# Kernel optimization log

Hardware: AMD Instinct MI355X
Metric: run time of the kernel (lower is better)

Reference implementation:

```python
import jax, jax.numpy as jnp
import numpy as np

B = 131072
INPUT_SIZE = 128
HIDDEN_SIZE = 128


def setup_inputs() -> dict:
    key = jax.random.key(0)
    ks = jax.random.split(key, 11)
    stdv = 1.0 / (HIDDEN_SIZE ** 0.5)

    def unif(k, shape):
        return jax.random.uniform(k, shape, dtype=jnp.float32, minval=-stdv, maxval=stdv)

    return {
        "x_t": jax.random.normal(ks[0], (B, INPUT_SIZE), dtype=jnp.float32),
        "h_prev": jax.random.normal(ks[1], (B, HIDDEN_SIZE), dtype=jnp.float32),
        "Wz": unif(ks[2], (INPUT_SIZE, HIDDEN_SIZE)),
        "Uz": unif(ks[3], (HIDDEN_SIZE, HIDDEN_SIZE)),
        "bz": unif(ks[4], (HIDDEN_SIZE,)),
        "Wr": unif(ks[5], (INPUT_SIZE, HIDDEN_SIZE)),
        "Ur": unif(ks[6], (HIDDEN_SIZE, HIDDEN_SIZE)),
        "br": unif(ks[7], (HIDDEN_SIZE,)),
        "Wh": unif(ks[8], (INPUT_SIZE, HIDDEN_SIZE)),
        "Uh": unif(ks[9], (HIDDEN_SIZE, HIDDEN_SIZE)),
        "bh": unif(ks[10], (HIDDEN_SIZE,)),
    }


def reference(x_t, h_prev, Wz, Uz, bz, Wr, Ur, br, Wh, Uh, bh):
    # Fuse the three input-side and two hidden-side GEMMs by concatenating weights.
    W = jnp.concatenate([Wz, Wr, Wh], axis=1)        # [I, 3H]
    U = jnp.concatenate([Uz, Ur], axis=1)            # [H, 2H]
    xw = x_t @ W                                     # [B, 3H]
    hu = h_prev @ U                                  # [B, 2H]
    H = bz.shape[0]
    z_t = jax.nn.sigmoid(xw[:, :H] + hu[:, :H] + bz)
    r_t = jax.nn.sigmoid(xw[:, H:2 * H] + hu[:, H:] + br)
    h_cand = jnp.tanh(xw[:, 2 * H:] + (r_t * h_prev) @ Uh + bh)
    h_t = (1.0 - z_t) * h_prev + z_t * h_cand
    return h_t
```

## Files before the change

kernel.cpp:

```cpp
#include <hip/hip_runtime.h>
#include <hip/hip_bf16.h>

typedef __attribute__((ext_vector_type(8))) short bf16x8;
typedef __attribute__((ext_vector_type(4))) float f32x4;

#define GRU_B 131072
#define BM 32
#define TPB 8
#define NBLK (GRU_B / (BM * TPB))

static __device__ __forceinline__ ushort f2bf(float f) {
  union { float f; unsigned u; } v; v.f = f;
  unsigned r = v.u + 0x7FFFu + ((v.u >> 16) & 1u);
  return (ushort)(r >> 16);
}
static __device__ __forceinline__ float bf2f(ushort u) {
  union { unsigned u; float f; } v; v.u = ((unsigned)u) << 16;
  return v.f;
}
static __device__ __forceinline__ unsigned pk2(float a, float b) {
  float2 t; t.x = a; t.y = b;
  __hip_bfloat162 r = __float22bfloat162_rn(t);
  union { __hip_bfloat162 b; unsigned u; } cv; cv.b = r;
  return cv.u;
}
static __device__ __forceinline__ float fsig(float x) {
  return __builtin_amdgcn_rcpf(1.0f + __expf(-x));
}
static __device__ __forceinline__ float ftanh(float x) {
  return 1.0f - 2.0f * __builtin_amdgcn_rcpf(1.0f + __expf(2.0f * x));
}
static __device__ __forceinline__ int swz(int row, int cbyte) {
  return (row * 256 + cbyte) ^ ((row & 7) << 4) ^ ((row & 8) << 2);
}

#define BARRIER() do {                                       \
  asm volatile("s_waitcnt lgkmcnt(0)" ::: "memory");         \
  __builtin_amdgcn_s_barrier();                              \
  asm volatile("" ::: "memory");                             \
} while (0)

__global__ void wtrans_kernel(const float* __restrict__ wz, const float* __restrict__ uz,
                              const float* __restrict__ wr, const float* __restrict__ ur,
                              const float* __restrict__ wh, const float* __restrict__ uh,
                              ushort* __restrict__ outw) {
  int f = blockIdx.x * 256 + threadIdx.x;
  int mat = f >> 14;
  int rem = f & 16383;
  int chunk = rem >> 9;
  int lane = (rem >> 3) & 63;
  int e = rem & 7;
  int cb = chunk >> 2, k0b = chunk & 3;
  int n = cb * 16 + (lane & 15);
  int k = k0b * 32 + (lane >> 4) * 8 + e;
  const float* src = (mat == 0) ? wz : (mat == 1) ? uz : (mat == 2) ? wr
                   : (mat == 3) ? ur : (mat == 4) ? wh : uh;
  outw[f] = f2bf(src[k * 128 + n]);
}

#define MFMA __builtin_amdgcn_mfma_f32_16x16x32_bf16

__global__ __launch_bounds__(512, 2) void gru_kernel(
    const float* __restrict__ x, const float* __restrict__ hprev,
    const ushort* __restrict__ wt,
    const float* __restrict__ bz, const float* __restrict__ br,
    const float* __restrict__ bh, float* __restrict__ out) {
  __shared__ __align__(16) char smem[65536];

  const int tid = threadIdx.x;
  const int lane = tid & 63;
  const int wid = tid >> 6;
  const int l15 = lane & 15;
  const int q = lane >> 4;
  const int n0 = wid * 16;

  const float4 brv = *(const float4*)(br + n0 + q * 4);
  const float4 bzv = *(const float4*)(bz + n0 + q * 4);
  const float4 bhv = *(const float4*)(bh + n0 + q * 4);
  const f32x4 brv4 = {brv.x, brv.y, brv.z, brv.w};
  const f32x4 bzv4 = {bzv.x, bzv.y, bzv.z, bzv.w};
  const f32x4 bhv4 = {bhv.x, bhv.y, bhv.z, bhv.w};

  const ushort* wlane = wt + (lane << 3);
  bf16x8 W[6][4];
#pragma unroll
  for (int mat = 0; mat < 6; ++mat)
#pragma unroll
    for (int kb = 0; kb < 4; ++kb)
      W[mat][kb] = *(const bf16x8*)(wlane + ((((mat << 3) + wid) << 2) + kb) * 512);

  auto ldsA = [&](const char* base, int mr, int k0) -> bf16x8 {
    int row = mr * 16 + l15;
    return *(const bf16x8*)(base + swz(row, (k0 + q * 8) * 2));
  };

  const long tile0 = (long)blockIdx.x * TPB;
  const float4* xg = (const float4*)x;
  const float4* hg = (const float4*)hprev;

  const int r0 = tid >> 5, cb0 = (tid & 31) << 3;
  const int bo0 = swz(r0, cb0), bo1 = swz(r0 + 16, cb0);
  const int go0 = swz(l15, (n0 + q * 4) * 2);
  const int go1 = swz(16 + l15, (n0 + q * 4) * 2);

  auto stage = [&](char* S, const float4& a0, const float4& a1,
                   const float4& b0, const float4& b1) {
    uint2 v;
    v.x = pk2(a0.x, a0.y); v.y = pk2(a0.z, a0.w); *(uint2*)(S + bo0) = v;
    v.x = pk2(a1.x, a1.y); v.y = pk2(a1.z, a1.w); *(uint2*)(S + bo1) = v;
    v.x = pk2(b0.x, b0.y); v.y = pk2(b0.z, b0.w); *(uint2*)(S + 8192 + bo0) = v;
    v.x = pk2(b1.x, b1.y); v.y = pk2(b1.z, b1.w); *(uint2*)(S + 8192 + bo1) = v;
  };

  float4 px0, px1, ph0, ph1;
  {
    long toff = tile0 * 1024;
    px0 = xg[toff + tid]; px1 = xg[toff + 512 + tid];
    ph0 = hg[toff + tid]; ph1 = hg[toff + 512 + tid];
    stage(smem, px0, px1, ph0, ph1);
    if (TPB > 1) {
      toff += 1024;
      px0 = xg[toff + tid]; px1 = xg[toff + 512 + tid];
      ph0 = hg[toff + tid]; ph1 = hg[toff + 512 + tid];
    }
  }
  BARRIER();

  for (int t = 0; t < TPB; ++t) {
    char* Scur = smem + (t % 3) * 16384;
    char* RHc  = smem + 49152 + (t & 1) * 8192;
    const long row0 = (tile0 + t) * BM;

    if (t + 1 < TPB) stage(smem + ((t + 1) % 3) * 16384, px0, px1, ph0, ph1);

    if (t + 2 < TPB) {
      long toff = (tile0 + t + 2) * 1024;
      px0 = xg[toff + tid]; px1 = xg[toff + 512 + tid];
      ph0 = hg[toff + tid]; ph1 = hg[toff + 512 + tid];
    }

    f32x4 accr[2], accz[2], acch[2];
    accr[0] = brv4; accr[1] = brv4;
    accz[0] = bzv4; accz[1] = bzv4;
    acch[0] = bhv4; acch[1] = bhv4;
    __builtin_amdgcn_s_setprio(1);
#pragma unroll
    for (int kb = 0; kb < 4; ++kb)
#pragma unroll
      for (int mr = 0; mr < 2; ++mr) {
        bf16x8 ax = ldsA(Scur, mr, kb * 32);
        bf16x8 ah = ldsA(Scur + 8192, mr, kb * 32);
        accr[mr] = MFMA(W[2][kb], ax, accr[mr], 0, 0, 0);
        accr[mr] = MFMA(W[3][kb], ah, accr[mr], 0, 0, 0);
        accz[mr] = MFMA(W[0][kb], ax, accz[mr], 0, 0, 0);
        accz[mr] = MFMA(W[1][kb], ah, accz[mr], 0, 0, 0);
        acch[mr] = MFMA(W[4][kb], ax, acch[mr], 0, 0, 0);
      }
    __builtin_amdgcn_s_setprio(0);

    uint2 hpk[2];
#pragma unroll
    for (int mr = 0; mr < 2; ++mr) {
      int go = mr ? go1 : go0;
      uint2 hp4 = *(const uint2*)(Scur + 8192 + go);
      hpk[mr] = hp4;
      float h0 = bf2f((ushort)(hp4.x & 0xffff)), h1 = bf2f((ushort)(hp4.x >> 16));
      float h2 = bf2f((ushort)(hp4.y & 0xffff)), h3 = bf2f((ushort)(hp4.y >> 16));
      uint2 w;
      w.x = pk2(fsig(accr[mr][0]) * h0, fsig(accr[mr][1]) * h1);
      w.y = pk2(fsig(accr[mr][2]) * h2, fsig(accr[mr][3]) * h3);
      *(uint2*)(RHc + go) = w;
    }

    BARRIER();

    __builtin_amdgcn_s_setprio(1);
#pragma unroll
    for (int kb = 0; kb < 4; ++kb)
#pragma unroll
      for (int mr = 0; mr < 2; ++mr)
        acch[mr] = MFMA(W[5][kb], ldsA(RHc, mr, kb * 32), acch[mr], 0, 0, 0);
    __builtin_amdgcn_s_setprio(0);

#pragma unroll
    for (int mr = 0; mr < 2; ++mr) {
      float hpf[4];
      hpf[0] = bf2f((ushort)(hpk[mr].x & 0xffff));
      hpf[1] = bf2f((ushort)(hpk[mr].x >> 16));
      hpf[2] = bf2f((ushort)(hpk[mr].y & 0xffff));
      hpf[3] = bf2f((ushort)(hpk[mr].y >> 16));
      float4 v;
#pragma unroll
      for (int j = 0; j < 4; ++j) {
        float hc = ftanh(acch[mr][j]);
        float zv = fsig(accz[mr][j]);
        ((float*)&v)[j] = hpf[j] + zv * (hc - hpf[j]);
      }
      *(float4*)(out + (row0 + mr * 16 + l15) * 128 + n0 + q * 4) = v;
    }
  }
}

extern "C" void kernel_launch(void* const* d_in, const int* in_sizes, int n_in,
                              void* d_out, int out_size, void* d_ws, size_t ws_size,
                              hipStream_t stream) {
  const float* x  = (const float*)d_in[0];
  const float* h  = (const float*)d_in[1];
  const float* Wz = (const float*)d_in[2];
  const float* Uz = (const float*)d_in[3];
  const float* bz = (const float*)d_in[4];
  const float* Wr = (const float*)d_in[5];
  const float* Ur = (const float*)d_in[6];
  const float* br = (const float*)d_in[7];
  const float* Wh = (const float*)d_in[8];
  const float* Uh = (const float*)d_in[9];
  const float* bh = (const float*)d_in[10];
  ushort* wt = (ushort*)d_ws;

  hipLaunchKernelGGL(wtrans_kernel, dim3(384), dim3(256), 0, stream,
                     Wz, Uz, Wr, Ur, Wh, Uh, wt);
  hipLaunchKernelGGL(gru_kernel, dim3(NBLK), dim3(512), 0, stream,
                     x, h, wt, bz, br, bh, (float*)d_out);
}
```

Measured before the change: 52.79 us.

## Stream weight fragments from global per tile and halve tiles per block

Stops holding all 24 bf16 weight fragments in registers for the whole block. Each tile now reloads its weight fragments from global memory (expected to hit L2/L1), which frees many VGPRs. Tiles per block drop from 8 to 4, so there are twice as many blocks, and the staging ring shrinks from triple to double buffering, cutting LDS from 64KB to 48KB. The aim is more overlap and occupancy, at the price of repeated weight loads inside the MFMA loop that can add latency. The double buffer may also add write-after-read hazards on the staging slots.

```diff
diff --git a/kernel.cpp b/kernel.cpp
--- a/kernel.cpp
+++ b/kernel.cpp
@@ -6,7 +6,7 @@
 
 #define GRU_B 131072
 #define BM 32
-#define TPB 8
+#define TPB 4
 #define NBLK (GRU_B / (BM * TPB))
 
 static __device__ __forceinline__ ushort f2bf(float f) {
@@ -65,7 +65,7 @@
     const ushort* __restrict__ wt,
     const float* __restrict__ bz, const float* __restrict__ br,
     const float* __restrict__ bh, float* __restrict__ out) {
-  __shared__ __align__(16) char smem[65536];
+  __shared__ __align__(16) char smem[49152];
 
   const int tid = threadIdx.x;
   const int lane = tid & 63;
@@ -82,12 +82,9 @@
   const f32x4 bhv4 = {bhv.x, bhv.y, bhv.z, bhv.w};
 
   const ushort* wlane = wt + (lane << 3);
-  bf16x8 W[6][4];
-#pragma unroll
-  for (int mat = 0; mat < 6; ++mat)
-#pragma unroll
-    for (int kb = 0; kb < 4; ++kb)
-      W[mat][kb] = *(const bf16x8*)(wlane + ((((mat << 3) + wid) << 2) + kb) * 512);
+  auto wfrag = [&](int mat, int kb) -> const bf16x8* {
+    return (const bf16x8*)(wlane + ((((mat << 3) + wid) << 2) + kb) * 512);
+  };
 
   auto ldsA = [&](const char* base, int mr, int k0) -> bf16x8 {
     int row = mr * 16 + l15;
@@ -127,11 +124,11 @@
   BARRIER();
 
   for (int t = 0; t < TPB; ++t) {
-    char* Scur = smem + (t % 3) * 16384;
-    char* RHc  = smem + 49152 + (t & 1) * 8192;
+    char* Scur = smem + (t & 1) * 16384;
+    char* RHc  = smem + 32768 + (t & 1) * 8192;
     const long row0 = (tile0 + t) * BM;
 
-    if (t + 1 < TPB) stage(smem + ((t + 1) % 3) * 16384, px0, px1, ph0, ph1);
+    if (t + 1 < TPB) stage(smem + ((t + 1) & 1) * 16384, px0, px1, ph0, ph1);
 
     if (t + 2 < TPB) {
       long toff = (tile0 + t + 2) * 1024;
@@ -145,17 +142,23 @@
     acch[0] = bhv4; acch[1] = bhv4;
     __builtin_amdgcn_s_setprio(1);
 #pragma unroll
-    for (int kb = 0; kb < 4; ++kb)
+    for (int kb = 0; kb < 4; ++kb) {
+      bf16x8 bWz = *wfrag(0, kb);
+      bf16x8 bUz = *wfrag(1, kb);
+      bf16x8 bWr = *wfrag(2, kb);
+      bf16x8 bUr = *wfrag(3, kb);
+      bf16x8 bWh = *wfrag(4, kb);
 #pragma unroll
       for (int mr = 0; mr < 2; ++mr) {
         bf16x8 ax = ldsA(Scur, mr, kb * 32);
         bf16x8 ah = ldsA(Scur + 8192, mr, kb * 32);
-        accr[mr] = MFMA(W[2][kb], ax, accr[mr], 0, 0, 0);
-        accr[mr] = MFMA(W[3][kb], ah, accr[mr], 0, 0, 0);
-        accz[mr] = MFMA(W[0][kb], ax, accz[mr], 0, 0, 0);
-        accz[mr] = MFMA(W[1][kb], ah, accz[mr], 0, 0, 0);
-        acch[mr] = MFMA(W[4][kb], ax, acch[mr], 0, 0, 0);
+        accr[mr] = MFMA(bWr, ax, accr[mr], 0, 0, 0);
+        accr[mr] = MFMA(bUr, ah, accr[mr], 0, 0, 0);
+        accz[mr] = MFMA(bWz, ax, accz[mr], 0, 0, 0);
+        accz[mr] = MFMA(bUz, ah, accz[mr], 0, 0, 0);
+        acch[mr] = MFMA(bWh, ax, acch[mr], 0, 0, 0);
       }
+    }
     __builtin_amdgcn_s_setprio(0);
 
     uint2 hpk[2];
@@ -176,10 +179,12 @@
 
     __builtin_amdgcn_s_setprio(1);
 #pragma unroll
-    for (int kb = 0; kb < 4; ++kb)
+    for (int kb = 0; kb < 4; ++kb) {
+      bf16x8 bUh = *wfrag(5, kb);
 #pragma unroll
       for (int mr = 0; mr < 2; ++mr)
-        acch[mr] = MFMA(W[5][kb], ldsA(RHc, mr, kb * 32), acch[mr], 0, 0, 0);
+        acch[mr] = MFMA(bUh, ldsA(RHc, mr, kb * 32), acch[mr], 0, 0, 0);
+    }
     __builtin_amdgcn_s_setprio(0);
 
 #pragma unroll
```

After: 62.83 us. +19.0%, slower.
